# Performance work log

Hardware: AMD Instinct MI355X
Metric: run time of the kernel (lower is better)

Reference implementation:

```python
import jax, jax.numpy as jnp
import numpy as np

B, N, F_IN, H, F = 2, 2048, 128, 8, 32  # FH = 256, a has 2F = 64


def setup_inputs() -> dict:
    key = jax.random.key(0)
    k_g, k_x, k_w, k_a = jax.random.split(key, 4)
    # sparse-ish adjacency with self loops (float mask, as in the keras code)
    u = jax.random.uniform(k_g, (B, N, N), dtype=jnp.float32)
    g = jnp.maximum((u < 0.05).astype(jnp.float32), jnp.eye(N, dtype=jnp.float32)[None])
    x = jax.random.normal(k_x, (B, N, F_IN), dtype=jnp.float32)
    w = jax.random.normal(k_w, (F_IN, F * H), dtype=jnp.float32) * (1.0 / np.sqrt(F_IN))
    a = jax.random.normal(k_a, (2 * F,), dtype=jnp.float32) * 0.1
    return {"g": g, "x": x, "w": w, "a": a, "n_heads": H}


def reference(g, x, w, a, n_heads):
    # g: [B,N,N] adjacency, x: [B,N,F_in], w: [F_in, F*H], a: [2F]
    Bd, Nd, _ = g.shape
    Fh = w.shape[1] // n_heads
    # linear transform + split heads: xh[b,n,h,f] == (x@w)[b,n, f + Fh*h]
    xh = jnp.dot(x, w).reshape(Bd, Nd, n_heads, Fh)  # [B,N,H,F]
    a1, a2 = a[:Fh], a[Fh:]
    # concat-attention is linear: score[b,i,j,h] = a1.x_j + a2.x_i
    s_j = jnp.einsum('bnhf,f->bnh', xh, a1)  # contribution of the tiled-over-axis1 copy (_x1 -> node j)
    s_i = jnp.einsum('bnhf,f->bnh', xh, a2)  # contribution of _x2 -> node i
    scores = s_i[:, :, None, :] + s_j[:, None, :, :]  # [B,N,N,H]
    e = jnp.exp(jax.nn.leaky_relu(scores, negative_slope=0.2))
    # normalize by sum over neighbors j masked by adjacency (keepdims like K.sum(..., keepdims=True))
    norm = jnp.sum(e * g[..., None], axis=2, keepdims=True)  # [B,N,1,H]
    return e / norm
```

## Files before the change

kernel.cpp:

```cpp
#include <hip/hip_runtime.h>

constexpr int Bv  = 2;
constexpr int Nv  = 2048;
constexpr int FIN = 128;
constexpr int Hn  = 8;
constexpr int Fv  = 32;
constexpr int NROW = Bv * Nv;
constexpr int S    = NROW * Hn;

typedef float v4f __attribute__((ext_vector_type(4)));

__global__ __launch_bounds__(256) void prep_kernel(
    const float* __restrict__ w, const float* __restrict__ a,
    const float* __restrict__ x, float* __restrict__ pq) {
    __shared__ float wa[2 * FIN * Hn];
    const int tid = threadIdx.x;

    for (int e = tid; e < 2 * FIN * Hn; e += 256) {
        const int which = e >> 10;
        const int k     = (e >> 3) & (FIN - 1);
        const int h     = e & (Hn - 1);
        const float* ap = a + which * Fv;
        const float* wp = w + (size_t)k * (Fv * Hn) + h * Fv;
        float s = 0.f;
        #pragma unroll
        for (int f = 0; f < Fv; ++f) s = fmaf(wp[f], ap[f], s);
        wa[e] = s;
    }
    __syncthreads();

    const int row = blockIdx.x * 32 + (tid >> 3);
    const int h   = tid & (Hn - 1);
    const float* xr = x + (size_t)row * FIN;
    float sj = 0.f, si = 0.f;
    #pragma unroll 4
    for (int k = 0; k < FIN; ++k) {
        const float xv = xr[k];
        sj = fmaf(xv, wa[k * Hn + h], sj);
        si = fmaf(xv, wa[FIN * Hn + k * Hn + h], si);
    }
    const int idx = row * Hn + h;
    pq[idx]         = __expf(sj);
    pq[S + idx]     = __expf(0.2f * sj);
    pq[2 * S + idx] = __expf(si);
    pq[3 * S + idx] = __expf(0.2f * si);
}

__global__ __launch_bounds__(256) void norm_kernel(
    const float* __restrict__ g, const float* __restrict__ pq,
    float* __restrict__ tbl) {
    const int row  = blockIdx.x;
    const int b    = row >> 11;
    const int tid  = threadIdx.x;
    const int lane = tid & 63, wv = tid >> 6;

    __shared__ int   idxs[Nv];
    __shared__ int   wavesum[4];
    __shared__ int   base_s;
    __shared__ float red[4][Hn];

    if (tid == 0) base_s = 0;
    __syncthreads();

    const float* __restrict__ grow = g + (size_t)row * Nv;

    for (int c = 0; c < Nv / 256; ++c) {
        const int j = c * 256 + tid;
        const bool pred = grow[j] != 0.f;
        const unsigned long long m = __ballot(pred);
        if (lane == 0) wavesum[wv] = __popcll(m);
        __syncthreads();
        int woff = base_s;
        #pragma unroll
        for (int w2 = 0; w2 < 4; ++w2) if (w2 < wv) woff += wavesum[w2];
        const int total = wavesum[0] + wavesum[1] + wavesum[2] + wavesum[3];
        if (pred)
            idxs[woff + __popcll(m & ((1ull << lane) - 1))] = j;
        __syncthreads();
        if (tid == 0) base_s += total;
    }
    __syncthreads();
    const int cnt = base_s;

    float pi[Hn], qi[Hn];
    #pragma unroll
    for (int h = 0; h < Hn; ++h) {
        pi[h] = pq[2 * S + row * Hn + h];
        qi[h] = pq[3 * S + row * Hn + h];
    }
    const float4* __restrict__ Pj4 = (const float4*)(pq + (size_t)b * Nv * Hn);
    const float4* __restrict__ Qj4 = (const float4*)(pq + S + (size_t)b * Nv * Hn);

    float acc[Hn];
    #pragma unroll
    for (int h = 0; h < Hn; ++h) acc[h] = 0.f;

    for (int t = tid; t < cnt; t += 256) {
        const int jj = idxs[t];
        const float4 p0 = Pj4[2 * jj], p1 = Pj4[2 * jj + 1];
        const float4 q0 = Qj4[2 * jj], q1 = Qj4[2 * jj + 1];
        acc[0] += fmaxf(pi[0] * p0.x, qi[0] * q0.x);
        acc[1] += fmaxf(pi[1] * p0.y, qi[1] * q0.y);
        acc[2] += fmaxf(pi[2] * p0.z, qi[2] * q0.z);
        acc[3] += fmaxf(pi[3] * p0.w, qi[3] * q0.w);
        acc[4] += fmaxf(pi[4] * p1.x, qi[4] * q1.x);
        acc[5] += fmaxf(pi[5] * p1.y, qi[5] * q1.y);
        acc[6] += fmaxf(pi[6] * p1.z, qi[6] * q1.z);
        acc[7] += fmaxf(pi[7] * p1.w, qi[7] * q1.w);
    }

    #pragma unroll
    for (int h = 0; h < Hn; ++h) {
        float v = acc[h];
        #pragma unroll
        for (int off = 32; off > 0; off >>= 1) v += __shfl_down(v, off);
        if (lane == 0) red[wv][h] = v;
    }
    __syncthreads();
    if (tid < Hn) {
        const float nsum = red[0][tid] + red[1][tid] + red[2][tid] + red[3][tid];
        const float rn = 1.0f / nsum;
        const float piv = pq[2 * S + row * Hn + tid];
        const float qiv = pq[3 * S + row * Hn + tid];
        tbl[row * 16 + tid]     = piv * rn;
        tbl[row * 16 + 8 + tid] = qiv * rn;
    }
}

constexpr int RPB = 8;
constexpr int SPB = 1024;

__global__ __launch_bounds__(256) void out_kernel(
    const float* __restrict__ pq, const float* __restrict__ tbl,
    float* __restrict__ out) {
    const int bid  = blockIdx.x;
    const int sg   = bid & 3;
    const int rg   = bid >> 2;
    const int row0 = rg * RPB;
    const int b    = row0 >> 11;
    const int tid  = threadIdx.x;
    const int hh   = tid & 1;

    const float4* __restrict__ Pb = (const float4*)(pq + (size_t)b * Nv * Hn);
    const float4* __restrict__ Qb = (const float4*)(pq + S + (size_t)b * Nv * Hn);

    float4 pjv[4], qjv[4];
    #pragma unroll
    for (int k = 0; k < 4; ++k) {
        const int s = sg * SPB + k * 256 + tid;
        pjv[k] = Pb[s];
        qjv[k] = Qb[s];
    }

    #pragma unroll
    for (int r = 0; r < RPB; ++r) {
        const int row = row0 + r;
        const float4 prv = *(const float4*)(tbl + row * 16 + hh * 4);
        const float4 qrv = *(const float4*)(tbl + row * 16 + 8 + hh * 4);
        float4* __restrict__ orow = (float4*)(out + (size_t)row * Nv * Hn);
        #pragma unroll
        for (int k = 0; k < 4; ++k) {
            const int s = sg * SPB + k * 256 + tid;
            float4 o;
            o.x = fmaxf(prv.x * pjv[k].x, qrv.x * qjv[k].x);
            o.y = fmaxf(prv.y * pjv[k].y, qrv.y * qjv[k].y);
            o.z = fmaxf(prv.z * pjv[k].z, qrv.z * qjv[k].z);
            o.w = fmaxf(prv.w * pjv[k].w, qrv.w * qjv[k].w);
            orow[s] = o;
        }
    }
}

extern "C" void kernel_launch(void* const* d_in, const int* in_sizes, int n_in,
                              void* d_out, int out_size, void* d_ws, size_t ws_size,
                              hipStream_t stream) {
    const float* g = (const float*)d_in[0];
    const float* x = (const float*)d_in[1];
    const float* w = (const float*)d_in[2];
    const float* a = (const float*)d_in[3];

    float* pq  = (float*)d_ws;
    float* tbl = pq + 4 * S;
    float* out = (float*)d_out;

    prep_kernel<<<NROW / 32, 256, 0, stream>>>(w, a, x, pq);
    norm_kernel<<<NROW, 256, 0, stream>>>(g, pq, tbl);
    out_kernel<<<(NROW / RPB) * 4, 256, 0, stream>>>(pq, tbl, out);
}
```

Measured before the change: 88.81 us.

## Vectorize adjacency compaction in norm kernel and stage x in shared memory for prep

The norm kernel now loads each adjacency row with two float4 loads per thread up front. It compacts neighbour indices in two ballot passes instead of eight scalar passes, which cuts the number of block barriers and load round trips per row. The prep kernel stages 16 rows of x in shared memory with vectorized loads and splits the K reduction across thread pairs, combined with a shuffle. This doubles the block count for better occupancy. Neighbour index order inside each chunk changes, so the summation order of the normalizer changes slightly.

After: 78.91 us. 1.13x faster.

```diff
diff --git a/kernel.cpp b/kernel.cpp
--- a/kernel.cpp
+++ b/kernel.cpp
@@ -8,13 +8,15 @@
 constexpr int NROW = Bv * Nv;
 constexpr int S    = NROW * Hn;
 
-typedef float v4f __attribute__((ext_vector_type(4)));
+constexpr int PREP_RPB = 16;
 
 __global__ __launch_bounds__(256) void prep_kernel(
     const float* __restrict__ w, const float* __restrict__ a,
     const float* __restrict__ x, float* __restrict__ pq) {
     __shared__ float wa[2 * FIN * Hn];
-    const int tid = threadIdx.x;
+    __shared__ float xs[PREP_RPB][FIN];
+    const int tid  = threadIdx.x;
+    const int row0 = blockIdx.x * PREP_RPB;
 
     for (int e = tid; e < 2 * FIN * Hn; e += 256) {
         const int which = e >> 10;
@@ -27,23 +29,40 @@
         for (int f = 0; f < Fv; ++f) s = fmaf(wp[f], ap[f], s);
         wa[e] = s;
     }
+
+    {
+        float4* xs4 = (float4*)&xs[0][0];
+        const float4* xg = (const float4*)(x + (size_t)row0 * FIN);
+        #pragma unroll
+        for (int i = tid; i < PREP_RPB * FIN / 4; i += 256) xs4[i] = xg[i];
+    }
     __syncthreads();
 
-    const int row = blockIdx.x * 32 + (tid >> 3);
-    const int h   = tid & (Hn - 1);
-    const float* xr = x + (size_t)row * FIN;
+    const int r    = tid >> 4;
+    const int rem  = tid & 15;
+    const int h    = rem >> 1;
+    const int half = rem & 1;
+    const int k0   = half * 64;
+
     float sj = 0.f, si = 0.f;
-    #pragma unroll 4
-    for (int k = 0; k < FIN; ++k) {
-        const float xv = xr[k];
-        sj = fmaf(xv, wa[k * Hn + h], sj);
-        si = fmaf(xv, wa[FIN * Hn + k * Hn + h], si);
-    }
-    const int idx = row * Hn + h;
-    pq[idx]         = __expf(sj);
-    pq[S + idx]     = __expf(0.2f * sj);
-    pq[2 * S + idx] = __expf(si);
-    pq[3 * S + idx] = __expf(0.2f * si);
+    #pragma unroll 8
+    for (int k = 0; k < 64; ++k) {
+        const int kk = k0 + k;
+        const float xv = xs[r][kk];
+        sj = fmaf(xv, wa[kk * Hn + h], sj);
+        si = fmaf(xv, wa[FIN * Hn + kk * Hn + h], si);
+    }
+    sj += __shfl_xor(sj, 1);
+    si += __shfl_xor(si, 1);
+
+    if (half == 0) {
+        const int row = row0 + r;
+        const int idx = row * Hn + h;
+        pq[idx]         = __expf(sj);
+        pq[S + idx]     = __expf(0.2f * sj);
+        pq[2 * S + idx] = __expf(si);
+        pq[3 * S + idx] = __expf(0.2f * si);
+    }
 }
 
 __global__ __launch_bounds__(256) void norm_kernel(
@@ -60,27 +79,10 @@
     __shared__ float red[4][Hn];
 
     if (tid == 0) base_s = 0;
-    __syncthreads();
-
-    const float* __restrict__ grow = g + (size_t)row * Nv;
-
-    for (int c = 0; c < Nv / 256; ++c) {
-        const int j = c * 256 + tid;
-        const bool pred = grow[j] != 0.f;
-        const unsigned long long m = __ballot(pred);
-        if (lane == 0) wavesum[wv] = __popcll(m);
-        __syncthreads();
-        int woff = base_s;
-        #pragma unroll
-        for (int w2 = 0; w2 < 4; ++w2) if (w2 < wv) woff += wavesum[w2];
-        const int total = wavesum[0] + wavesum[1] + wavesum[2] + wavesum[3];
-        if (pred)
-            idxs[woff + __popcll(m & ((1ull << lane) - 1))] = j;
-        __syncthreads();
-        if (tid == 0) base_s += total;
-    }
-    __syncthreads();
-    const int cnt = base_s;
+
+    const float4* __restrict__ g4 = (const float4*)(g + (size_t)row * Nv);
+    const float4 gva = g4[tid];
+    const float4 gvb = g4[tid + 256];
 
     float pi[Hn], qi[Hn];
     #pragma unroll
@@ -88,6 +90,58 @@
         pi[h] = pq[2 * S + row * Hn + h];
         qi[h] = pq[3 * S + row * Hn + h];
     }
+
+    const unsigned long long below = (1ull << lane) - 1ull;
+
+    {
+        const float4 gv = gva;
+        const int j0 = 4 * tid;
+        const unsigned long long m0 = __ballot(gv.x != 0.f);
+        const unsigned long long m1 = __ballot(gv.y != 0.f);
+        const unsigned long long m2 = __ballot(gv.z != 0.f);
+        const unsigned long long m3 = __ballot(gv.w != 0.f);
+        if (lane == 0)
+            wavesum[wv] = __popcll(m0) + __popcll(m1) + __popcll(m2) + __popcll(m3);
+        __syncthreads();
+        int off = base_s;
+        #pragma unroll
+        for (int w2 = 0; w2 < 4; ++w2) if (w2 < wv) off += wavesum[w2];
+        const int total = wavesum[0] + wavesum[1] + wavesum[2] + wavesum[3];
+        off += __popcll(m0 & below) + __popcll(m1 & below)
+             + __popcll(m2 & below) + __popcll(m3 & below);
+        if (gv.x != 0.f) idxs[off++] = j0;
+        if (gv.y != 0.f) idxs[off++] = j0 + 1;
+        if (gv.z != 0.f) idxs[off++] = j0 + 2;
+        if (gv.w != 0.f) idxs[off++] = j0 + 3;
+        __syncthreads();
+        if (tid == 0) base_s += total;
+    }
+    {
+        const float4 gv = gvb;
+        const int j0 = 1024 + 4 * tid;
+        const unsigned long long m0 = __ballot(gv.x != 0.f);
+        const unsigned long long m1 = __ballot(gv.y != 0.f);
+        const unsigned long long m2 = __ballot(gv.z != 0.f);
+        const unsigned long long m3 = __ballot(gv.w != 0.f);
+        if (lane == 0)
+            wavesum[wv] = __popcll(m0) + __popcll(m1) + __popcll(m2) + __popcll(m3);
+        __syncthreads();
+        int off = base_s;
+        #pragma unroll
+        for (int w2 = 0; w2 < 4; ++w2) if (w2 < wv) off += wavesum[w2];
+        const int total = wavesum[0] + wavesum[1] + wavesum[2] + wavesum[3];
+        off += __popcll(m0 & below) + __popcll(m1 & below)
+             + __popcll(m2 & below) + __popcll(m3 & below);
+        if (gv.x != 0.f) idxs[off++] = j0;
+        if (gv.y != 0.f) idxs[off++] = j0 + 1;
+        if (gv.z != 0.f) idxs[off++] = j0 + 2;
+        if (gv.w != 0.f) idxs[off++] = j0 + 3;
+        __syncthreads();
+        if (tid == 0) base_s += total;
+    }
+    __syncthreads();
+    const int cnt = base_s;
+
     const float4* __restrict__ Pj4 = (const float4*)(pq + (size_t)b * Nv * Hn);
     const float4* __restrict__ Qj4 = (const float4*)(pq + S + (size_t)b * Nv * Hn);
 
@@ -183,7 +237,7 @@
     float* tbl = pq + 4 * S;
     float* out = (float*)d_out;
 
-    prep_kernel<<<NROW / 32, 256, 0, stream>>>(w, a, x, pq);
+    prep_kernel<<<NROW / PREP_RPB, 256, 0, stream>>>(w, a, x, pq);
     norm_kernel<<<NROW, 256, 0, stream>>>(g, pq, tbl);
     out_kernel<<<(NROW / RPB) * 4, 256, 0, stream>>>(pq, tbl, out);
 }
```
